# Optimization experiments

Measured on AMD Instinct MI355X. Metric: run time of the kernel, lower is better.

The kernel has to match this reference:

```python
import jax, jax.numpy as jnp
import numpy as np
from jax import lax

TAU = 2.0
V_TH = 1.0
ALPHA = 4.0   # spikingjelly surrogate.Sigmoid default
BN_EPS = 1e-5
HEADS = 8


def lif(x):
    """Multi-step LIF neuron (tau=2, v_reset=0, hard reset, detach_reset).
    x: [T, ...] -> spikes [T, ...]. Forward is Heaviside; sigmoid surrogate
    is wired in via straight-through for the bwd variant."""
    def step(v, xt):
        v = v + (xt - v) / TAU                      # charge
        sg = jax.nn.sigmoid(ALPHA * (v - V_TH))     # surrogate
        hard = (v >= V_TH).astype(x.dtype)
        spike = sg + lax.stop_gradient(hard - sg)   # fwd: hard, bwd: sigmoid'
        v = v * (1.0 - lax.stop_gradient(spike))    # detached hard reset to 0
        return v, spike
    _, s = lax.scan(step, jnp.zeros_like(x[0]), x)
    return s


def conv1x1_bn(x, w, g, b, m, var, bias=None):
    # x: [N, C, H, W]; 1x1 conv == channel matmul, then eval-mode BN
    y = jnp.einsum('nchw,dc->ndhw', x, w)
    if bias is not None:
        y = y + bias[None, :, None, None]
    scale = g / jnp.sqrt(var + BN_EPS)
    shift = b - m * scale
    return y * scale[None, :, None, None] + shift[None, :, None, None]


def to_heads(x, T, B, C, H, W):
    # [T,B,C,H,W] -> [T,B,heads,N,hd]
    N = H * W
    hd = C // HEADS
    x = x.reshape(T, B, C, N).transpose(0, 1, 3, 2)          # [T,B,N,C]
    return x.reshape(T, B, N, HEADS, hd).transpose(0, 1, 3, 2, 4)


def _forward(x, q_w, q_bn_g, q_bn_b, q_bn_m, q_bn_v,
             k_w, k_bn_g, k_bn_b, k_bn_m, k_bn_v,
             v_w, v_bn_g, v_bn_b, v_bn_m, v_bn_v,
             out_w, out_b, out_bn_g, out_bn_b, out_bn_m, out_bn_v):
    T, B, C, H, W = x.shape
    N = H * W
    identity = x

    xs = lif(x)                                  # shortcut_lif
    x_qkv = xs.reshape(T * B, C, H, W)

    q = lif(conv1x1_bn(x_qkv, q_w, q_bn_g, q_bn_b, q_bn_m, q_bn_v).reshape(T, B, C, H, W))
    k = lif(conv1x1_bn(x_qkv, k_w, k_bn_g, k_bn_b, k_bn_m, k_bn_v).reshape(T, B, C, H, W))
    v = lif(conv1x1_bn(x_qkv, v_w, v_bn_g, v_bn_b, v_bn_m, v_bn_v).reshape(T, B, C, H, W))

    qh = to_heads(q, T, B, C, H, W)              # [T,B,h,N,hd]
    kh = to_heads(k, T, B, C, H, W)
    vh = to_heads(v, T, B, C, H, W)

    kv = jnp.sum(kh * vh, axis=-2, keepdims=True)   # [T,B,h,1,hd]
    kv = lif(kv)                                    # talking_heads_proj_lif
    y = qh * kv                                     # [T,B,h,N,hd]

    # [T,B,h,N,hd] -> transpose(3,4) -> [T,B,h,hd,N] -> [T,B,C,H,W]
    y = y.transpose(0, 1, 2, 4, 3).reshape(T, B, C, H, W)
    y = conv1x1_bn(y.reshape(T * B, C, H, W), out_w, out_bn_g, out_bn_b,
                   out_bn_m, out_bn_v, bias=out_b).reshape(T, B, C, H, W)
    return y + identity, vh


def setup_inputs() -> dict:
    key = jax.random.key(0)
    ks = jax.random.split(key, 6)
    T, B, C, H, W = 4, 32, 512, 14, 14
    inp = {
        'x': jax.random.normal(ks[0], (T, B, C, H, W), dtype=jnp.float32),
        'q_w': jax.random.normal(ks[1], (C, C), dtype=jnp.float32) * 0.05,
        'k_w': jax.random.normal(ks[2], (C, C), dtype=jnp.float32) * 0.05,
        'v_w': jax.random.normal(ks[3], (C, C), dtype=jnp.float32) * 0.05,
        'out_w': jax.random.normal(ks[4], (C, C), dtype=jnp.float32) * 0.05,
        'out_b': jnp.zeros((C,), dtype=jnp.float32),
    }
    for p in ('q', 'k', 'v', 'out'):
        inp[f'{p}_bn_g'] = jnp.ones((C,), dtype=jnp.float32)
        inp[f'{p}_bn_b'] = jnp.zeros((C,), dtype=jnp.float32)
        inp[f'{p}_bn_m'] = jnp.zeros((C,), dtype=jnp.float32)
        inp[f'{p}_bn_v'] = jnp.ones((C,), dtype=jnp.float32)
    return inp


def reference(x, q_w, q_bn_g, q_bn_b, q_bn_m, q_bn_v,
              k_w, k_bn_g, k_bn_b, k_bn_m, k_bn_v,
              v_w, v_bn_g, v_bn_b, v_bn_m, v_bn_v,
              out_w, out_b, out_bn_g, out_bn_b, out_bn_m, out_bn_v):
    return _forward(x, q_w, q_bn_g, q_bn_b, q_bn_m, q_bn_v,
                    k_w, k_bn_g, k_bn_b, k_bn_m, k_bn_v,
                    v_w, v_bn_g, v_bn_b, v_bn_m, v_bn_v,
                    out_w, out_b, out_bn_g, out_bn_b, out_bn_m, out_bn_v)
```

## Files before the change

### kernel.cpp

```cpp
#include <hip/hip_runtime.h>
#include <math.h>

#define T_   4
#define B_   32
#define C_   512
#define N_   196
#define TB_  128
#define M_   25088
#define BNP_ 6272
#define OUT1_ 12845056

typedef unsigned short ushort_t;
typedef __attribute__((ext_vector_type(8)))  __bf16 bf16x8;
typedef __attribute__((ext_vector_type(16))) float  f32x16;

__device__ __forceinline__ ushort_t f2bf(float f) {
    unsigned int u = __float_as_uint(f);
    u = u + 0x7FFFu + ((u >> 16) & 1u);
    return (ushort_t)(u >> 16);
}
__device__ __forceinline__ float bf2f(ushort_t h) {
    return __uint_as_float(((unsigned int)h) << 16);
}

#define GL2LDS(gp, lp) \
    __builtin_amdgcn_global_load_lds((const __attribute__((address_space(1))) void*)(gp), \
                                     (__attribute__((address_space(3))) void*)(lp), 16, 0, 0)

__global__ void prep_kernel(
    const float* __restrict__ qw, const float* __restrict__ kw,
    const float* __restrict__ vw, const float* __restrict__ ow,
    const float* __restrict__ qg, const float* __restrict__ qb, const float* __restrict__ qm, const float* __restrict__ qv,
    const float* __restrict__ kg, const float* __restrict__ kb, const float* __restrict__ km, const float* __restrict__ kvr,
    const float* __restrict__ vg, const float* __restrict__ vb, const float* __restrict__ vm, const float* __restrict__ vv,
    const float* __restrict__ og, const float* __restrict__ ob, const float* __restrict__ om, const float* __restrict__ ov,
    const float* __restrict__ obias,
    ushort_t* __restrict__ wsplit, ushort_t* __restrict__ osplit,
    float* __restrict__ scale_qkv, float* __restrict__ shift_qkv,
    float* __restrict__ scale_o,   float* __restrict__ shift_o,
    float* __restrict__ kvpart)
{
    int i = blockIdx.x * 256 + threadIdx.x;
    int d = i >> 9, c = i & 511;
    const float* src = (d < 512) ? qw : (d < 1024) ? kw : vw;
    float wv = src[(d & 511) * 512 + c];
    ushort_t h = f2bf(wv);
    float r1 = wv - bf2f(h);
    ushort_t mm = f2bf(r1);
    wsplit[((size_t)d * 2 + 0) * 512 + c] = h;
    wsplit[((size_t)d * 2 + 1) * 512 + c] = mm;
    if (d < 512)
        osplit[(size_t)d * 512 + c] = f2bf(ow[d * 512 + c]);

    if (i < 3 * C_) {
        int p = i >> 9, dl = i & 511;
        const float* g = (p == 0) ? qg : (p == 1) ? kg : vg;
        const float* b = (p == 0) ? qb : (p == 1) ? kb : vb;
        const float* m = (p == 0) ? qm : (p == 1) ? km : vm;
        const float* r = (p == 0) ? qv : (p == 1) ? kvr : vv;
        float sc = g[dl] / sqrtf(r[dl] + 1e-5f);
        scale_qkv[i] = sc;
        shift_qkv[i] = b[dl] - m[dl] * sc;
    }
    if (i < C_) {
        float sc = og[i] / sqrtf(ov[i] + 1e-5f);
        scale_o[i] = sc;
        shift_o[i] = ob[i] - om[i] * sc + obias[i] * sc;
    }
    if (i < TB_ * C_) kvpart[i] = 0.f;
}

__global__ __launch_bounds__(256)
void lifx_kernel(const float* __restrict__ x, ushort_t* __restrict__ xs)
{
    __shared__ ushort_t tile[64 * 66];
    const int tid = threadIdx.x;
    const int b = blockIdx.z, c0 = blockIdx.y * 64, n0 = blockIdx.x * 64;
    const int j = tid & 63, w = tid >> 6;
    const bool nok = (n0 + j) < N_;
    float v[16];
#pragma unroll
    for (int r = 0; r < 16; ++r) v[r] = 0.f;
    for (int t = 0; t < T_; ++t) {
        const float* xb = x + ((size_t)((t * B_ + b) * C_ + c0)) * N_ + n0 + j;
#pragma unroll
        for (int r = 0; r < 16; ++r) {
            int i = w * 16 + r;
            float xv = nok ? xb[(size_t)i * N_] : 0.f;
            v[r] = v[r] + (xv - v[r]) * 0.5f;
            bool s = (v[r] >= 1.0f);
            tile[j * 66 + i] = s ? 0x3F80 : 0;
            if (s) v[r] = 0.f;
        }
        __syncthreads();
#pragma unroll
        for (int p = 0; p < 2; ++p) {
            int w2 = tid + p * 256;
            int jj = w2 >> 3, ck = w2 & 7;
            if (n0 + jj < N_) {
                const unsigned int* src = reinterpret_cast<const unsigned int*>(&tile[jj * 66 + ck * 8]);
                uint4 dv; dv.x = src[0]; dv.y = src[1]; dv.z = src[2]; dv.w = src[3];
                size_t mp = (size_t)(b * N_ + n0 + jj) * 4 + t;
                *reinterpret_cast<uint4*>(&xs[mp * 512 + c0 + ck * 8]) = dv;
            }
        }
        __syncthreads();
    }
}

__global__ __launch_bounds__(512, 4)
void qkv_gemm_lif(const ushort_t* __restrict__ W, const ushort_t* __restrict__ X,
                  const float* __restrict__ scale, const float* __restrict__ shift,
                  ushort_t* __restrict__ spk, float* __restrict__ out2)
{
    const int id = blockIdx.x;
    const int xw = id & 7, local = id >> 3;
    const int ml = local / 12, d_t = local - ml * 12;
    const int m_t = ml * 8 + xw;
    if (m_t >= 98) return;
    const int m0 = m_t * 256;
    const int d0 = d_t * 128;

    __shared__ ushort_t Xs[2][16 * 512];
    __shared__ ushort_t Ws[2][16 * 512];
    const int tid = threadIdx.x, wid = tid >> 6, lane = tid & 63;
    const int mw = (wid & 3) * 64, dw = (wid >> 2) * 64;
    const int row32 = lane & 31, khalf = lane >> 5;

    f32x16 acc[2][2] = {};

    auto STAGE = [&](int buf, int k0) {
        {   int q = wid, mb = q >> 1, ks = q & 1;
            const ushort_t* g = X + (size_t)(m0 + mb * 32 + row32) * 512 + k0 + ks * 16 + khalf * 8;
            GL2LDS(g, &Xs[buf][q * 512]);
        }
        {   int q = wid + 8, mb = q >> 1, ks = q & 1;
            const ushort_t* g = X + (size_t)(m0 + mb * 32 + row32) * 512 + k0 + ks * 16 + khalf * 8;
            GL2LDS(g, &Xs[buf][q * 512]);
        }
        {   int q = wid, s = q >> 3, rem = q & 7, db = rem >> 1, ks = rem & 1;
            const ushort_t* g = W + ((size_t)(d0 + db * 32 + row32) * 2 + s) * 512 + k0 + ks * 16 + khalf * 8;
            GL2LDS(g, &Ws[buf][q * 512]);
        }
        {   int q = wid + 8, s = q >> 3, rem = q & 7, db = rem >> 1, ks = rem & 1;
            const ushort_t* g = W + ((size_t)(d0 + db * 32 + row32) * 2 + s) * 512 + k0 + ks * 16 + khalf * 8;
            GL2LDS(g, &Ws[buf][q * 512]);
        }
    };

    STAGE(0, 0);
    int cur = 0;

    for (int it = 0; it < 16; ++it) {
        if (it < 15) {
            STAGE(cur ^ 1, (it + 1) * 32);
            asm volatile("s_waitcnt vmcnt(4)" ::: "memory");
        } else {
            asm volatile("s_waitcnt vmcnt(0)" ::: "memory");
        }
        __builtin_amdgcn_s_barrier();
        __builtin_amdgcn_sched_barrier(0);

        __builtin_amdgcn_s_setprio(1);
#pragma unroll
        for (int ks = 0; ks < 2; ++ks) {
            bf16x8 xfr[2];
#pragma unroll
            for (int i = 0; i < 2; ++i)
                xfr[i] = *reinterpret_cast<const bf16x8*>(
                    &Xs[cur][(((mw >> 5) + i) * 2 + ks) * 512 + lane * 8]);
#pragma unroll
            for (int s = 0; s < 2; ++s)
#pragma unroll
                for (int j = 0; j < 2; ++j) {
                    bf16x8 wfr = *reinterpret_cast<const bf16x8*>(
                        &Ws[cur][(s * 8 + ((dw >> 5) + j) * 2 + ks) * 512 + lane * 8]);
#pragma unroll
                    for (int i = 0; i < 2; ++i)
                        acc[i][j] = __builtin_amdgcn_mfma_f32_32x32x16_bf16(xfr[i], wfr, acc[i][j], 0, 0, 0);
                }
        }
        __builtin_amdgcn_s_setprio(0);

        asm volatile("s_waitcnt lgkmcnt(0)" ::: "memory");
        __builtin_amdgcn_s_barrier();
        cur ^= 1;
    }

    const int p = d0 >> 9;
    const bool isV = (p == 2);
    ushort_t* plane = spk + (size_t)p * ((size_t)M_ * 512);
#pragma unroll
    for (int j = 0; j < 2; ++j) {
        int d = d0 + dw + j * 32 + row32;
        float sc = scale[d], sh = shift[d];
        int dl = d & 511;
        int h = dl >> 6, hd = dl & 63;
#pragma unroll
        for (int i = 0; i < 2; ++i) {
            int bnb = (m0 + mw + i * 32) >> 2;
            f32x16 a = acc[i][j];
#pragma unroll
            for (int g = 0; g < 4; ++g) {
                int bn = bnb + 2 * g + khalf;
                float p0 = fmaf(a[4 * g + 0], sc, sh);
                float p1 = fmaf(a[4 * g + 1], sc, sh);
                float p2 = fmaf(a[4 * g + 2], sc, sh);
                float p3 = fmaf(a[4 * g + 3], sc, sh);
                float v = p0 * 0.5f;
                bool s0 = (v >= 1.f); if (s0) v = 0.f;
                v = v + (p1 - v) * 0.5f;
                bool s1 = (v >= 1.f); if (s1) v = 0.f;
                v = v + (p2 - v) * 0.5f;
                bool s2 = (v >= 1.f); if (s2) v = 0.f;
                v = v + (p3 - v) * 0.5f;
                bool s3 = (v >= 1.f);
                ushort_t* b0 = plane + (size_t)bn * 512 + dl;
                b0[0]                      = s0 ? 0x3F80 : 0;
                b0[(size_t)BNP_ * 512]     = s1 ? 0x3F80 : 0;
                b0[(size_t)2 * BNP_ * 512] = s2 ? 0x3F80 : 0;
                b0[(size_t)3 * BNP_ * 512] = s3 ? 0x3F80 : 0;
                if (isV) {
                    int b = bn / N_, n = bn - b * N_;
                    float* o = out2 + (((size_t)b * 8 + h) * N_ + n) * 64 + hd;
                    o[0]                       = s0 ? 1.f : 0.f;
                    o[(size_t)1 * (OUT1_ / 4)] = s1 ? 1.f : 0.f;
                    o[(size_t)2 * (OUT1_ / 4)] = s2 ? 1.f : 0.f;
                    o[(size_t)3 * (OUT1_ / 4)] = s3 ? 1.f : 0.f;
                }
            }
        }
    }
}

__global__ __launch_bounds__(256)
void kv_part_kernel(const ushort_t* __restrict__ ks, const ushort_t* __restrict__ vs,
                    float* __restrict__ kvpart)
{
    __shared__ int cnt[256];
    const int tid = threadIdx.x;
    cnt[tid] = 0;
    __syncthreads();
    const int tb = blockIdx.x >> 1, ch = blockIdx.x & 1;
    const int cg = tid & 31, ns = tid >> 5;
    const int c = ch * 256 + cg * 8;
    const ushort_t* kb = ks + (size_t)tb * N_ * 512 + c;
    const ushort_t* vb = vs + (size_t)tb * N_ * 512 + c;
    int loc[8] = {0, 0, 0, 0, 0, 0, 0, 0};
    int n1 = ns * 25 + 25; if (n1 > N_) n1 = N_;
    for (int n = ns * 25; n < n1; ++n) {
        uint4 kq = *reinterpret_cast<const uint4*>(&kb[(size_t)n * 512]);
        uint4 vq = *reinterpret_cast<const uint4*>(&vb[(size_t)n * 512]);
        unsigned m;
        m = kq.x & vq.x; loc[0] += (m & 0xFFFFu) ? 1 : 0; loc[1] += (m >> 16) ? 1 : 0;
        m = kq.y & vq.y; loc[2] += (m & 0xFFFFu) ? 1 : 0; loc[3] += (m >> 16) ? 1 : 0;
        m = kq.z & vq.z; loc[4] += (m & 0xFFFFu) ? 1 : 0; loc[5] += (m >> 16) ? 1 : 0;
        m = kq.w & vq.w; loc[6] += (m & 0xFFFFu) ? 1 : 0; loc[7] += (m >> 16) ? 1 : 0;
    }
#pragma unroll
    for (int e = 0; e < 8; ++e) atomicAdd(&cnt[cg * 8 + e], loc[e]);
    __syncthreads();
    kvpart[tb * 512 + ch * 256 + tid] = (float)cnt[tid];
}

__global__ void kv_lif_kernel(const float* __restrict__ kvpart, ushort_t* __restrict__ kvs)
{
    int i = blockIdx.x * 256 + threadIdx.x;
    if (i >= B_ * C_) return;
    int b = i >> 9, c = i & 511;
    float v = 0.f;
#pragma unroll
    for (int t = 0; t < T_; ++t) {
        float y = kvpart[((t * B_ + b) << 9) + c];
        v = v + (y - v) * 0.5f;
        bool s = (v >= 1.f);
        kvs[((t * B_ + b) << 9) + c] = s ? 0x3F80 : 0;
        if (s) v = 0.f;
    }
}

__global__ __launch_bounds__(256)
void out_gemm(const ushort_t* __restrict__ A, const ushort_t* __restrict__ qs,
              const ushort_t* __restrict__ kvs,
              const float* __restrict__ scale, const float* __restrict__ shift,
              const float* __restrict__ xid, float* __restrict__ out)
{
    const int id = blockIdx.x;
    const int xw = id & 7, local = id >> 3;
    const int m_t = (local >> 2) * 8 + xw, d_t = local & 3;
    if (m_t >= 196) return;
    const int m0 = m_t * 128, d0 = d_t * 128;

    __shared__ ushort_t As[2][8 * 512];
    __shared__ ushort_t Bs[2][8 * 512];
    const int tid = threadIdx.x, wid = tid >> 6, lane = tid & 63;
    const int dw = (wid >> 1) * 64, mw = (wid & 1) * 64;
    const int row32 = lane & 31, khalf = lane >> 5;

    int sm[2], stb[2], sq[2], sL[2];
#pragma unroll
    for (int u = 0; u < 2; ++u) {
        int s = tid + u * 256;
        sq[u] = s >> 6; sL[u] = s & 63;
        sm[u] = m0 + (sq[u] >> 1) * 32 + (sL[u] & 31);
        stb[u] = sm[u] / N_;
    }

    f32x16 acc[2][2] = {};

    {
        uint4 o[2];
#pragma unroll
        for (int u = 0; u < 2; ++u) {
            int kk = (sq[u] & 1) * 16 + (sL[u] >> 5) * 8;
            uint4 qv = *reinterpret_cast<const uint4*>(&qs[(size_t)sm[u] * 512 + kk]);
            uint4 kv = *reinterpret_cast<const uint4*>(&kvs[(size_t)stb[u] * 512 + kk]);
            o[u].x = qv.x & kv.x; o[u].y = qv.y & kv.y;
            o[u].z = qv.z & kv.z; o[u].w = qv.w & kv.w;
        }
        for (int q = wid; q < 8; q += 4) {
            int db = q >> 1, ks2 = q & 1;
            const ushort_t* g = A + (size_t)(d0 + db * 32 + row32) * 512 + ks2 * 16 + khalf * 8;
            GL2LDS(g, &As[0][q * 512]);
        }
#pragma unroll
        for (int u = 0; u < 2; ++u)
            *reinterpret_cast<uint4*>(&Bs[0][sq[u] * 512 + sL[u] * 8]) = o[u];
    }
    __syncthreads();

    int buf = 0;
    for (int it = 0; it < 16; ++it) {
        uint4 nq[2], nk[2];
        if (it < 15) {
            int k0n = (it + 1) * 32;
#pragma unroll
            for (int u = 0; u < 2; ++u) {
                int kk = k0n + (sq[u] & 1) * 16 + (sL[u] >> 5) * 8;
                nq[u] = *reinterpret_cast<const uint4*>(&qs[(size_t)sm[u] * 512 + kk]);
                nk[u] = *reinterpret_cast<const uint4*>(&kvs[(size_t)stb[u] * 512 + kk]);
            }
            for (int q = wid; q < 8; q += 4) {
                int db = q >> 1, ks2 = q & 1;
                const ushort_t* g = A + (size_t)(d0 + db * 32 + row32) * 512 + k0n + ks2 * 16 + khalf * 8;
                GL2LDS(g, &As[buf ^ 1][q * 512]);
            }
        }

        __builtin_amdgcn_s_setprio(1);
#pragma unroll
        for (int ks = 0; ks < 2; ++ks) {
            bf16x8 afr[2];
#pragma unroll
            for (int i = 0; i < 2; ++i)
                afr[i] = *reinterpret_cast<const bf16x8*>(
                    &As[buf][(((dw >> 5) + i) * 2 + ks) * 512 + lane * 8]);
#pragma unroll
            for (int j = 0; j < 2; ++j) {
                bf16x8 bfr = *reinterpret_cast<const bf16x8*>(
                    &Bs[buf][(((mw >> 5) + j) * 2 + ks) * 512 + lane * 8]);
#pragma unroll
                for (int i = 0; i < 2; ++i)
                    acc[i][j] = __builtin_amdgcn_mfma_f32_32x32x16_bf16(afr[i], bfr, acc[i][j], 0, 0, 0);
            }
        }
        __builtin_amdgcn_s_setprio(0);

        if (it < 15) {
#pragma unroll
            for (int u = 0; u < 2; ++u) {
                uint4 o;
                o.x = nq[u].x & nk[u].x; o.y = nq[u].y & nk[u].y;
                o.z = nq[u].z & nk[u].z; o.w = nq[u].w & nk[u].w;
                *reinterpret_cast<uint4*>(&Bs[buf ^ 1][sq[u] * 512 + sL[u] * 8]) = o;
            }
        }
        __syncthreads();
        buf ^= 1;
    }

#pragma unroll
    for (int j = 0; j < 2; ++j) {
        int m = m0 + mw + j * 32 + row32;
        int tb = m / N_;
        int n  = m - tb * N_;
        size_t mbase = (size_t)tb * (C_ * N_) + n;
#pragma unroll
        for (int i = 0; i < 2; ++i) {
            int dbase = d0 + dw + i * 32 + 4 * khalf;
            f32x16 a = acc[i][j];
#pragma unroll
            for (int g = 0; g < 4; ++g) {
#pragma unroll
                for (int t = 0; t < 4; ++t) {
                    int d = dbase + t + 8 * g;
                    float val = fmaf(a[4 * g + t], scale[d], shift[d]);
                    size_t ad = mbase + (size_t)d * N_;
                    out[ad] = val + xid[ad];
                }
            }
        }
    }
}

extern "C" void kernel_launch(void* const* d_in, const int* in_sizes, int n_in,
                              void* d_out, int out_size, void* d_ws, size_t ws_size,
                              hipStream_t stream)
{
    const float* x    = (const float*)d_in[0];
    const float* q_w  = (const float*)d_in[1];
    const float* k_w  = (const float*)d_in[2];
    const float* v_w  = (const float*)d_in[3];
    const float* o_w  = (const float*)d_in[4];
    const float* o_b  = (const float*)d_in[5];
    const float* qg = (const float*)d_in[6],  *qb = (const float*)d_in[7],
               *qm = (const float*)d_in[8],  *qv = (const float*)d_in[9];
    const float* kg = (const float*)d_in[10], *kb = (const float*)d_in[11],
               *km = (const float*)d_in[12], *kv = (const float*)d_in[13];
    const float* vg = (const float*)d_in[14], *vb = (const float*)d_in[15],
               *vm = (const float*)d_in[16], *vv = (const float*)d_in[17];
    const float* og = (const float*)d_in[18], *ob = (const float*)d_in[19],
               *om = (const float*)d_in[20], *ov = (const float*)d_in[21];

    float* out1  = (float*)d_out;
    float* out2f = out1 + OUT1_;

    ushort_t* spk    = (ushort_t*)d_ws;
    ushort_t* xs     = spk + (size_t)3 * M_ * 512;
    ushort_t* wsplit = xs + (size_t)M_ * 512;
    ushort_t* osplit = wsplit + (size_t)1536 * 2 * 512;
    float*    kvpart = (float*)(osplit + (size_t)512 * 512);
    ushort_t* kvs    = (ushort_t*)(kvpart + TB_ * C_);
    float*    scq    = (float*)(kvs + TB_ * C_);
    float*    shq    = scq + 3 * C_;
    float*    sco    = shq + 3 * C_;
    float*    sho    = sco + C_;

    ushort_t* qsp = spk;
    ushort_t* ksp = spk + (size_t)M_ * 512;
    ushort_t* vsp = spk + (size_t)2 * M_ * 512;

    prep_kernel<<<(1536 * 512) / 256, 256, 0, stream>>>(
        q_w, k_w, v_w, o_w,
        qg, qb, qm, qv, kg, kb, km, kv, vg, vb, vm, vv, og, ob, om, ov, o_b,
        wsplit, osplit, scq, shq, sco, sho, kvpart);

    lifx_kernel<<<dim3(4, 8, 32), 256, 0, stream>>>(x, xs);

    qkv_gemm_lif<<<1200, 512, 0, stream>>>(wsplit, xs, scq, shq, spk, out2f);

    kv_part_kernel<<<256, 256, 0, stream>>>(ksp, vsp, kvpart);

    kv_lif_kernel<<<64, 256, 0, stream>>>(kvpart, kvs);

    out_gemm<<<800, 256, 0, stream>>>(osplit, qsp, kvs, sco, sho, x, out1);
}
```

Baseline: 407.0 us.

## Load QKV GEMM MFMA operands directly from global memory instead of LDS staging

Drops the double-buffered LDS staging (global-to-LDS copies, waitcnts and barriers) in the QKV GEMM and has each wave load its bf16x8 X and W fragments straight from global memory into registers each k-step. This removes LDS traffic and block-wide synchronisation and frees LDS, which could raise occupancy. In exchange, operands shared across waves in a block are now fetched redundantly from L2/global, there is no explicit software prefetch, and the loop depends on the compiler to hide load latency.

New measurement: 531.9 us. 1.31x slower.

```diff
diff --git a/kernel.cpp b/kernel.cpp
--- a/kernel.cpp
+++ b/kernel.cpp
@@ -121,70 +121,50 @@
     const int m0 = m_t * 256;
     const int d0 = d_t * 128;
 
-    __shared__ ushort_t Xs[2][16 * 512];
-    __shared__ ushort_t Ws[2][16 * 512];
     const int tid = threadIdx.x, wid = tid >> 6, lane = tid & 63;
     const int mw = (wid & 3) * 64, dw = (wid >> 2) * 64;
     const int row32 = lane & 31, khalf = lane >> 5;
 
+    unsigned xo[2][2];
+    unsigned wo[2][2][2];
+#pragma unroll
+    for (int i = 0; i < 2; ++i)
+#pragma unroll
+        for (int ks = 0; ks < 2; ++ks)
+            xo[i][ks] = (unsigned)((m0 + mw + i * 32 + row32) * 512 + ks * 16 + khalf * 8);
+#pragma unroll
+    for (int s = 0; s < 2; ++s)
+#pragma unroll
+        for (int j = 0; j < 2; ++j)
+#pragma unroll
+            for (int ks = 0; ks < 2; ++ks)
+                wo[s][j][ks] = (unsigned)(((d0 + dw + j * 32 + row32) * 2 + s) * 512 + ks * 16 + khalf * 8);
+
     f32x16 acc[2][2] = {};
 
-    auto STAGE = [&](int buf, int k0) {
-        {   int q = wid, mb = q >> 1, ks = q & 1;
-            const ushort_t* g = X + (size_t)(m0 + mb * 32 + row32) * 512 + k0 + ks * 16 + khalf * 8;
-            GL2LDS(g, &Xs[buf][q * 512]);
-        }
-        {   int q = wid + 8, mb = q >> 1, ks = q & 1;
-            const ushort_t* g = X + (size_t)(m0 + mb * 32 + row32) * 512 + k0 + ks * 16 + khalf * 8;
-            GL2LDS(g, &Xs[buf][q * 512]);
-        }
-        {   int q = wid, s = q >> 3, rem = q & 7, db = rem >> 1, ks = rem & 1;
-            const ushort_t* g = W + ((size_t)(d0 + db * 32 + row32) * 2 + s) * 512 + k0 + ks * 16 + khalf * 8;
-            GL2LDS(g, &Ws[buf][q * 512]);
-        }
-        {   int q = wid + 8, s = q >> 3, rem = q & 7, db = rem >> 1, ks = rem & 1;
-            const ushort_t* g = W + ((size_t)(d0 + db * 32 + row32) * 2 + s) * 512 + k0 + ks * 16 + khalf * 8;
-            GL2LDS(g, &Ws[buf][q * 512]);
-        }
-    };
-
-    STAGE(0, 0);
-    int cur = 0;
-
-    for (int it = 0; it < 16; ++it) {
-        if (it < 15) {
-            STAGE(cur ^ 1, (it + 1) * 32);
-            asm volatile("s_waitcnt vmcnt(4)" ::: "memory");
-        } else {
-            asm volatile("s_waitcnt vmcnt(0)" ::: "memory");
-        }
-        __builtin_amdgcn_s_barrier();
-        __builtin_amdgcn_sched_barrier(0);
-
-        __builtin_amdgcn_s_setprio(1);
-#pragma unroll
-        for (int ks = 0; ks < 2; ++ks) {
-            bf16x8 xfr[2];
-#pragma unroll
-            for (int i = 0; i < 2; ++i)
-                xfr[i] = *reinterpret_cast<const bf16x8*>(
-                    &Xs[cur][(((mw >> 5) + i) * 2 + ks) * 512 + lane * 8]);
-#pragma unroll
-            for (int s = 0; s < 2; ++s)
-#pragma unroll
-                for (int j = 0; j < 2; ++j) {
-                    bf16x8 wfr = *reinterpret_cast<const bf16x8*>(
-                        &Ws[cur][(s * 8 + ((dw >> 5) + j) * 2 + ks) * 512 + lane * 8]);
+    for (int k0 = 0; k0 < 512; k0 += 32) {
+        bf16x8 xfr[2][2];
+#pragma unroll
+        for (int i = 0; i < 2; ++i)
+#pragma unroll
+            for (int ks = 0; ks < 2; ++ks)
+                xfr[i][ks] = *reinterpret_cast<const bf16x8*>(X + xo[i][ks] + k0);
+#pragma unroll
+        for (int s = 0; s < 2; ++s) {
+            bf16x8 wfr[2][2];
+#pragma unroll
+            for (int j = 0; j < 2; ++j)
+#pragma unroll
+                for (int ks = 0; ks < 2; ++ks)
+                    wfr[j][ks] = *reinterpret_cast<const bf16x8*>(W + wo[s][j][ks] + k0);
+#pragma unroll
+            for (int ks = 0; ks < 2; ++ks)
+#pragma unroll
+                for (int j = 0; j < 2; ++j)
 #pragma unroll
                     for (int i = 0; i < 2; ++i)
-                        acc[i][j] = __builtin_amdgcn_mfma_f32_32x32x16_bf16(xfr[i], wfr, acc[i][j], 0, 0, 0);
-                }
-        }
-        __builtin_amdgcn_s_setprio(0);
-
-        asm volatile("s_waitcnt lgkmcnt(0)" ::: "memory");
-        __builtin_amdgcn_s_barrier();
-        cur ^= 1;
+                        acc[i][j] = __builtin_amdgcn_mfma_f32_32x32x16_bf16(xfr[i][ks], wfr[j][ks], acc[i][j], 0, 0, 0);
+        }
     }
 
     const int p = d0 >> 9;
```
